# Optimization experiments

Measured on AMD Instinct MI355X. Metric: run time of the kernel, lower is better.

Reference implementation:

```python
import jax, jax.numpy as jnp
import numpy as np

B, N, CQ, CKV, CP = 4, 1024, 128, 64, 16
H, NB = 4, 3
D = CQ // H  # 32 per-head dim
NQ, NK = 32, 128
CENTRES = 15.5 + 32.0 * np.arange(N // NQ)  # subset centres covering all atoms


def _ln(x, eps=1e-5):
    m = jnp.mean(x, axis=-1, keepdims=True)
    v = jnp.var(x, axis=-1, keepdims=True)
    return (x - m) * jax.lax.rsqrt(v + eps)


def _adaln(a, s, s_gamma, w_gate, w_skip):
    # AF3 AdaLN: a normalized without affine, modulated by conditioning s
    a_n = _ln(a)
    s_n = _ln(s) * s_gamma
    return jax.nn.sigmoid(s_n @ w_gate) * a_n + s_n @ w_skip


def _local_bias():
    # sequence-local block mask (union over subset centres), Algorithm 7
    idx = jnp.arange(N, dtype=jnp.float32)
    cen = jnp.asarray(CENTRES, dtype=jnp.float32)
    lcond = jnp.abs(idx[None, :] - cen[:, None]) < NQ / 2  # [C, N] query window
    mcond = jnp.abs(idx[None, :] - cen[:, None]) < NK / 2  # [C, N] key window
    cond = jnp.any(lcond[:, :, None] & mcond[:, None, :], axis=0)  # [N, N]
    return jnp.where(cond, 0.0, -1e10)


def _forward(q, c, p, attn_s_gamma, attn_gate_w, attn_skip_w, attn_wq, attn_bq,
             attn_wk, attn_wv, attn_lnz_g, attn_lnz_b, attn_wb, attn_wgate,
             attn_wo, attn_ws_out, attn_bs_out, trans_s_gamma, trans_gate_w,
             trans_skip_w, trans_w1, trans_w2, trans_wout, trans_ws_out,
             trans_bs_out):
    beta = _local_bias()  # [N, N]
    inv_sqrt_d = 1.0 / np.sqrt(D)
    a = q
    for i in range(NB):  # 3 structurally distinct blocks
        # --- AttentionPairBias (AF3 Alg 24) ---
        ah = _adaln(a, c, attn_s_gamma[i], attn_gate_w[i], attn_skip_w[i])
        qh = (ah @ attn_wq[i] + attn_bq[i]).reshape(B, N, H, D)
        kh = (ah @ attn_wk[i]).reshape(B, N, H, D)
        vh = (ah @ attn_wv[i]).reshape(B, N, H, D)
        zb = (_ln(p) * attn_lnz_g[i] + attn_lnz_b[i]) @ attn_wb[i]  # [B,N,N,H]
        bias = jnp.transpose(zb, (0, 3, 1, 2)) + beta[None, None]  # [B,H,N,N]
        scores = jnp.einsum('bqhd,bkhd->bhqk', qh, kh) * inv_sqrt_d + bias
        w = jax.nn.softmax(scores, axis=-1)
        o = jnp.einsum('bhqk,bkhd->bqhd', w, vh)
        g = jax.nn.sigmoid((ah @ attn_wgate[i]).reshape(B, N, H, D))
        o = (g * o).reshape(B, N, CQ) @ attn_wo[i]
        attn_out = jax.nn.sigmoid(c @ attn_ws_out[i] + attn_bs_out[i]) * o
        # --- ConditionedTransitionBlock (AF3 Alg 25, n=2 SwiGLU) ---
        t = _adaln(a, c, trans_s_gamma[i], trans_gate_w[i], trans_skip_w[i])
        bm = jax.nn.silu(t @ trans_w1[i]) * (t @ trans_w2[i])
        t_out = jax.nn.sigmoid(c @ trans_ws_out[i] + trans_bs_out[i]) * (bm @ trans_wout[i])
        # AF3 Alg 23: a <- attn_out + transition(a, s)
        a = attn_out + t_out
    return a


def setup_inputs() -> dict:
    key = jax.random.key(0)
    ks = iter(jax.random.split(key, 64))

    def rnd(shape, scale=0.02):
        return jax.random.normal(next(ks), shape, dtype=jnp.float32) * scale

    return {
        'q': jax.random.normal(next(ks), (B, N, CQ), dtype=jnp.float32),
        'c': jax.random.normal(next(ks), (B, N, CKV), dtype=jnp.float32),
        'p': jax.random.normal(next(ks), (B, N, N, CP), dtype=jnp.float32),
        'attn_s_gamma': jnp.ones((NB, CKV), jnp.float32),
        'attn_gate_w': rnd((NB, CKV, CQ)),
        'attn_skip_w': rnd((NB, CKV, CQ)),
        'attn_wq': rnd((NB, CQ, CQ)),
        'attn_bq': jnp.zeros((NB, CQ), jnp.float32),
        'attn_wk': rnd((NB, CQ, CQ)),
        'attn_wv': rnd((NB, CQ, CQ)),
        'attn_lnz_g': jnp.ones((NB, CP), jnp.float32),
        'attn_lnz_b': jnp.zeros((NB, CP), jnp.float32),
        'attn_wb': rnd((NB, CP, H)),
        'attn_wgate': rnd((NB, CQ, CQ)),
        'attn_wo': rnd((NB, CQ, CQ)),
        'attn_ws_out': rnd((NB, CKV, CQ)),
        'attn_bs_out': jnp.full((NB, CQ), -2.0, jnp.float32),
        'trans_s_gamma': jnp.ones((NB, CKV), jnp.float32),
        'trans_gate_w': rnd((NB, CKV, CQ)),
        'trans_skip_w': rnd((NB, CKV, CQ)),
        'trans_w1': rnd((NB, CQ, 2 * CQ)),
        'trans_w2': rnd((NB, CQ, 2 * CQ)),
        'trans_wout': rnd((NB, 2 * CQ, CQ)),
        'trans_ws_out': rnd((NB, CKV, CQ)),
        'trans_bs_out': jnp.full((NB, CQ), -2.0, jnp.float32),
    }


def reference(q, c, p, attn_s_gamma, attn_gate_w, attn_skip_w, attn_wq, attn_bq,
              attn_wk, attn_wv, attn_lnz_g, attn_lnz_b, attn_wb, attn_wgate,
              attn_wo, attn_ws_out, attn_bs_out, trans_s_gamma, trans_gate_w,
              trans_skip_w, trans_w1, trans_w2, trans_wout, trans_ws_out,
              trans_bs_out):
    return _forward(q, c, p, attn_s_gamma, attn_gate_w, attn_skip_w, attn_wq,
                    attn_bq, attn_wk, attn_wv, attn_lnz_g, attn_lnz_b, attn_wb,
                    attn_wgate, attn_wo, attn_ws_out, attn_bs_out,
                    trans_s_gamma, trans_gate_w, trans_skip_w, trans_w1,
                    trans_w2, trans_wout, trans_ws_out, trans_bs_out)
```

## Files before the change

### kernel.cpp

```cpp
#include <hip/hip_runtime.h>
#include <math.h>

#define NB_ 3
#define B_ 4
#define N_ 1024
#define CQ_ 128
#define CKV_ 64
#define CP_ 16
#define H_ 4
#define D_ 32
#define R_ (B_*N_)
#define KW_ 128

__device__ __forceinline__ float sigmoidf_(float x) {
    return 1.0f / (1.0f + __expf(-x));
}

#define AN_OFF 0
#define SA_OFF 1056
#define ST_OFF 1600
#define CR_OFF 2144
#define TH_OFF 2688
#define SCR_OFF 3744
#define SMEM_F (3744 + 6336)

__global__ __launch_bounds__(512, 4) void k_pre(
    const float* __restrict__ a, const float* __restrict__ c,
    const float* __restrict__ a_sg, const float* __restrict__ a_gw,
    const float* __restrict__ a_sw, const float* __restrict__ a_wso,
    const float* __restrict__ a_bso,
    const float* __restrict__ t_sg, const float* __restrict__ t_gw,
    const float* __restrict__ t_sw, const float* __restrict__ t_wso,
    const float* __restrict__ t_bso,
    const float* __restrict__ wq, const float* __restrict__ bq,
    const float* __restrict__ wk, const float* __restrict__ wv,
    const float* __restrict__ wg,
    const float* __restrict__ w1, const float* __restrict__ w2,
    float* __restrict__ qh, float* __restrict__ kh,
    float* __restrict__ vh, float* __restrict__ gh,
    float* __restrict__ bm,
    float* __restrict__ asig, float* __restrict__ tsig)
{
    __shared__ float smem[SMEM_F];
    const int t = threadIdx.x;
    const int base = blockIdx.x * 8;

    {
        const int rloc = t >> 6, li = t & 63;
        const int row = base + rloc;
        float2 av = *(const float2*)(a + row * 128 + li * 2);
        float s = av.x + av.y;
        float ss = av.x * av.x + av.y * av.y;
        float cv = c[row * 64 + li];
        float cs = cv, css = cv * cv;
        #pragma unroll
        for (int m = 1; m < 64; m <<= 1) {
            s += __shfl_xor(s, m);
            ss += __shfl_xor(ss, m);
            cs += __shfl_xor(cs, m);
            css += __shfl_xor(css, m);
        }
        const float am = s * (1.0f / 128.0f);
        const float ars = rsqrtf(ss * (1.0f / 128.0f) - am * am + 1e-5f);
        const float cm = cs * (1.0f / 64.0f);
        const float crs = rsqrtf(css * (1.0f / 64.0f) - cm * cm + 1e-5f);
        smem[AN_OFF + rloc * 132 + li * 2]     = (av.x - am) * ars;
        smem[AN_OFF + rloc * 132 + li * 2 + 1] = (av.y - am) * ars;
        const float cn = (cv - cm) * crs;
        smem[SA_OFF + rloc * 68 + li] = cn * a_sg[li];
        smem[ST_OFF + rloc * 68 + li] = cn * t_sg[li];
        smem[CR_OFF + rloc * 68 + li] = cv;
    }
    __syncthreads();

    const int wave = t >> 6;
    const int lane = t & 63;
    const int ig = lane >> 4;
    const int jc = lane & 15;
    const int c0 = jc * 8;
    const int r0 = ig * 2, r1 = ig * 2 + 1;

    if (wave < 6) {
        const float* W;
        const float* xs;
        switch (wave) {
            case 0: W = a_gw;  xs = smem + SA_OFF; break;
            case 1: W = a_sw;  xs = smem + SA_OFF; break;
            case 2: W = t_gw;  xs = smem + ST_OFF; break;
            case 3: W = t_sw;  xs = smem + ST_OFF; break;
            case 4: W = a_wso; xs = smem + CR_OFF; break;
            default: W = t_wso; xs = smem + CR_OFF; break;
        }
        W += c0;
        float acc0[8], acc1[8];
        #pragma unroll
        for (int e = 0; e < 8; e++) { acc0[e] = 0.f; acc1[e] = 0.f; }
        for (int kk = 0; kk < 64; kk += 4) {
            float4 x40 = *(const float4*)(xs + r0 * 68 + kk);
            float4 x41 = *(const float4*)(xs + r1 * 68 + kk);
            #pragma unroll
            for (int q = 0; q < 4; q++) {
                const float4 wlo = *(const float4*)(W + (kk + q) * 128);
                const float4 whi = *(const float4*)(W + (kk + q) * 128 + 4);
                const float xa = ((const float*)&x40)[q];
                const float xb = ((const float*)&x41)[q];
                acc0[0] += xa * wlo.x; acc0[1] += xa * wlo.y;
                acc0[2] += xa * wlo.z; acc0[3] += xa * wlo.w;
                acc0[4] += xa * whi.x; acc0[5] += xa * whi.y;
                acc0[6] += xa * whi.z; acc0[7] += xa * whi.w;
                acc1[0] += xb * wlo.x; acc1[1] += xb * wlo.y;
                acc1[2] += xb * wlo.z; acc1[3] += xb * wlo.w;
                acc1[4] += xb * whi.x; acc1[5] += xb * whi.y;
                acc1[6] += xb * whi.z; acc1[7] += xb * whi.w;
            }
        }
        float* sc = smem + SCR_OFF + wave * 1056;
        *(float4*)(sc + r0 * 132 + c0)     = make_float4(acc0[0], acc0[1], acc0[2], acc0[3]);
        *(float4*)(sc + r0 * 132 + c0 + 4) = make_float4(acc0[4], acc0[5], acc0[6], acc0[7]);
        *(float4*)(sc + r1 * 132 + c0)     = make_float4(acc1[0], acc1[1], acc1[2], acc1[3]);
        *(float4*)(sc + r1 * 132 + c0 + 4) = make_float4(acc1[4], acc1[5], acc1[6], acc1[7]);
    }
    __syncthreads();

    #pragma unroll
    for (int i2 = 0; i2 < 2; i2++) {
        const int e = t + i2 * 512;
        const int r = e >> 7, cc = e & 127;
        const float* sc = smem + SCR_OFF + r * 132 + cc;
        const float anv = smem[AN_OFF + r * 132 + cc];
        const float ahv = sigmoidf_(sc[0]) * anv + sc[1056];
        const float thv = sigmoidf_(sc[2 * 1056]) * anv + sc[3 * 1056];
        smem[AN_OFF + r * 132 + cc] = ahv;
        smem[TH_OFF + r * 132 + cc] = thv;
        const int idx = (base + r) * 128 + cc;
        asig[idx] = sigmoidf_(sc[4 * 1056] + a_bso[cc]);
        tsig[idx] = sigmoidf_(sc[5 * 1056] + t_bso[cc]);
    }
    __syncthreads();

    {
        const float* W;
        const float* xs;
        int ldw, sel2 = 0, cb = 0;
        if (wave < 4) {
            W = (wave == 0 ? wq : wave == 1 ? wk : wave == 2 ? wv : wg) + c0;
            xs = smem + AN_OFF;
            ldw = 128;
        } else {
            const int u = (wave - 4) * 128 + c0;
            sel2 = u >> 8; cb = u & 255;
            W = (sel2 ? w2 : w1) + cb;
            xs = smem + TH_OFF;
            ldw = 256;
        }
        float acc0[8], acc1[8];
        #pragma unroll
        for (int e = 0; e < 8; e++) {
            const float init = (wave == 0) ? bq[c0 + e] : 0.f;
            acc0[e] = init; acc1[e] = init;
        }
        for (int kk = 0; kk < 128; kk += 4) {
            float4 x40 = *(const float4*)(xs + r0 * 132 + kk);
            float4 x41 = *(const float4*)(xs + r1 * 132 + kk);
            #pragma unroll
            for (int q = 0; q < 4; q++) {
                const float4 wlo = *(const float4*)(W + (kk + q) * ldw);
                const float4 whi = *(const float4*)(W + (kk + q) * ldw + 4);
                const float xa = ((const float*)&x40)[q];
                const float xb = ((const float*)&x41)[q];
                acc0[0] += xa * wlo.x; acc0[1] += xa * wlo.y;
                acc0[2] += xa * wlo.z; acc0[3] += xa * wlo.w;
                acc0[4] += xa * whi.x; acc0[5] += xa * whi.y;
                acc0[6] += xa * whi.z; acc0[7] += xa * whi.w;
                acc1[0] += xb * wlo.x; acc1[1] += xb * wlo.y;
                acc1[2] += xb * wlo.z; acc1[3] += xb * wlo.w;
                acc1[4] += xb * whi.x; acc1[5] += xb * whi.y;
                acc1[6] += xb * whi.z; acc1[7] += xb * whi.w;
            }
        }
        if (wave < 4) {
            float* dst = (wave == 0 ? qh : wave == 1 ? kh : wave == 2 ? vh : gh);
            if (wave == 3) {
                #pragma unroll
                for (int e = 0; e < 8; e++) {
                    acc0[e] = sigmoidf_(acc0[e]);
                    acc1[e] = sigmoidf_(acc1[e]);
                }
            }
            *(float4*)(dst + (base + r0) * 128 + c0)     = make_float4(acc0[0], acc0[1], acc0[2], acc0[3]);
            *(float4*)(dst + (base + r0) * 128 + c0 + 4) = make_float4(acc0[4], acc0[5], acc0[6], acc0[7]);
            *(float4*)(dst + (base + r1) * 128 + c0)     = make_float4(acc1[0], acc1[1], acc1[2], acc1[3]);
            *(float4*)(dst + (base + r1) * 128 + c0 + 4) = make_float4(acc1[4], acc1[5], acc1[6], acc1[7]);
        } else {
            float* bsc = smem + SCR_OFF + sel2 * 2080;
            *(float4*)(bsc + r0 * 260 + cb)     = make_float4(acc0[0], acc0[1], acc0[2], acc0[3]);
            *(float4*)(bsc + r0 * 260 + cb + 4) = make_float4(acc0[4], acc0[5], acc0[6], acc0[7]);
            *(float4*)(bsc + r1 * 260 + cb)     = make_float4(acc1[0], acc1[1], acc1[2], acc1[3]);
            *(float4*)(bsc + r1 * 260 + cb + 4) = make_float4(acc1[4], acc1[5], acc1[6], acc1[7]);
        }
    }
    __syncthreads();

    #pragma unroll
    for (int i2 = 0; i2 < 4; i2++) {
        const int e = t + i2 * 512;
        const int r = e >> 8, cc = e & 255;
        const float a1 = smem[SCR_OFF + r * 260 + cc];
        const float a2 = smem[SCR_OFF + 2080 + r * 260 + cc];
        bm[(base + r) * 256 + cc] = a1 * sigmoidf_(a1) * a2;
    }
}

__global__ __launch_bounds__(256) void k_zbias(
    const float* __restrict__ p,
    const float* __restrict__ lnz_g, const float* __restrict__ lnz_b,
    const float* __restrict__ wb, float* __restrict__ zb)
{
    const int tid = blockIdx.x * 256 + threadIdx.x;
    const int kk = tid & 127;
    const int n = (tid >> 7) & 1023;
    const int b = tid >> 17;
    const int row = b * N_ + n;
    const int k = ((n >> 5) << 5) - 48 + kk;

    if (k < 0 || k >= N_) {
        #pragma unroll
        for (int blk = 0; blk < NB_; blk++) {
            float* zo = zb + ((size_t)(blk * R_ + row) * H_) * KW_ + kk;
            #pragma unroll
            for (int h = 0; h < H_; h++) zo[h * KW_] = -1e10f;
        }
        return;
    }
    const float* pp = p + ((size_t)row * N_ + k) * CP_;
    float pv[16];
    float4 p0 = *(const float4*)(pp);
    float4 p1 = *(const float4*)(pp + 4);
    float4 p2 = *(const float4*)(pp + 8);
    float4 p3 = *(const float4*)(pp + 12);
    pv[0]=p0.x; pv[1]=p0.y; pv[2]=p0.z; pv[3]=p0.w;
    pv[4]=p1.x; pv[5]=p1.y; pv[6]=p1.z; pv[7]=p1.w;
    pv[8]=p2.x; pv[9]=p2.y; pv[10]=p2.z; pv[11]=p2.w;
    pv[12]=p3.x; pv[13]=p3.y; pv[14]=p3.z; pv[15]=p3.w;
    float s = 0.f, ss = 0.f;
    #pragma unroll
    for (int i = 0; i < 16; i++) { s += pv[i]; ss += pv[i] * pv[i]; }
    const float m = s * (1.0f / 16.0f);
    const float rs = rsqrtf(ss * (1.0f / 16.0f) - m * m + 1e-5f);

    #pragma unroll
    for (int blk = 0; blk < NB_; blk++) {
        const float* g = lnz_g + blk * 16;
        const float* bb = lnz_b + blk * 16;
        const float* w = wb + blk * 64;
        float z0 = 0.f, z1 = 0.f, z2 = 0.f, z3 = 0.f;
        #pragma unroll
        for (int cp = 0; cp < 16; cp++) {
            const float val = (pv[cp] - m) * rs * g[cp] + bb[cp];
            z0 += val * w[cp * 4 + 0];
            z1 += val * w[cp * 4 + 1];
            z2 += val * w[cp * 4 + 2];
            z3 += val * w[cp * 4 + 3];
        }
        float* zo = zb + ((size_t)(blk * R_ + row) * H_) * KW_ + kk;
        zo[0] = z0; zo[KW_] = z1; zo[2 * KW_] = z2; zo[3 * KW_] = z3;
    }
}

__global__ __launch_bounds__(256) void k_attn(
    const float* __restrict__ qh, const float* __restrict__ kh,
    const float* __restrict__ vh, const float* __restrict__ gh,
    const float* __restrict__ zb, float* __restrict__ og)
{
    __shared__ float kT[32][136];
    __shared__ float vs[128][36];
    __shared__ float wsm[32][132];

    const int t = threadIdx.x;
    const int qb = blockIdx.x, h = blockIdx.y, b = blockIdx.z;
    const int k0 = qb * 32 - 48;

    #pragma unroll
    for (int i = 0; i < 4; i++) {
        const int e = t + i * 256;
        const int kk = e >> 3, d4 = (e & 7) * 4;
        const int kg = k0 + kk;
        float4 kv = make_float4(0.f, 0.f, 0.f, 0.f);
        float4 vv = make_float4(0.f, 0.f, 0.f, 0.f);
        if (kg >= 0 && kg < N_) {
            const int addr = (b * N_ + kg) * 128 + h * 32 + d4;
            kv = *(const float4*)(kh + addr);
            vv = *(const float4*)(vh + addr);
        }
        kT[d4 + 0][kk] = kv.x;
        kT[d4 + 1][kk] = kv.y;
        kT[d4 + 2][kk] = kv.z;
        kT[d4 + 3][kk] = kv.w;
        *(float4*)&vs[kk][d4] = vv;
    }

    const int q = t >> 3, j = t & 7;
    const int n = qb * 32 + q;
    const float* qrow = qh + (b * N_ + n) * 128 + h * 32;
    float4 qf[8];
    #pragma unroll
    for (int dq = 0; dq < 8; dq++) qf[dq] = *(const float4*)(qrow + dq * 4);
    const float* zrow = zb + ((size_t)(b * N_ + n) * H_ + h) * KW_;
    float4 zf[4];
    #pragma unroll
    for (int g4 = 0; g4 < 4; g4++) zf[g4] = *(const float4*)(zrow + g4 * 32 + j * 4);
    __syncthreads();

    float4 acc[4];
    #pragma unroll
    for (int g4 = 0; g4 < 4; g4++) acc[g4] = make_float4(0.f, 0.f, 0.f, 0.f);
    const float* qfs = (const float*)qf;
    #pragma unroll
    for (int d = 0; d < 32; d++) {
        const float qd = qfs[d];
        #pragma unroll
        for (int g4 = 0; g4 < 4; g4++) {
            const float4 k4 = *(const float4*)&kT[d][g4 * 32 + j * 4];
            acc[g4].x += qd * k4.x; acc[g4].y += qd * k4.y;
            acc[g4].z += qd * k4.z; acc[g4].w += qd * k4.w;
        }
    }
    const float scale = 0.1767766952966369f;
    float fr[16];
    #pragma unroll
    for (int g4 = 0; g4 < 4; g4++) {
        fr[g4*4+0] = zf[g4].x + acc[g4].x * scale;
        fr[g4*4+1] = zf[g4].y + acc[g4].y * scale;
        fr[g4*4+2] = zf[g4].z + acc[g4].z * scale;
        fr[g4*4+3] = zf[g4].w + acc[g4].w * scale;
    }
    float mx = fr[0];
    #pragma unroll
    for (int i = 1; i < 16; i++) mx = fmaxf(mx, fr[i]);
    #pragma unroll
    for (int mk = 1; mk < 8; mk <<= 1) mx = fmaxf(mx, __shfl_xor(mx, mk));
    float sum = 0.f;
    #pragma unroll
    for (int i = 0; i < 16; i++) { fr[i] = __expf(fr[i] - mx); sum += fr[i]; }
    #pragma unroll
    for (int mk = 1; mk < 8; mk <<= 1) sum += __shfl_xor(sum, mk);
    const float rinv = 1.0f / sum;
    #pragma unroll
    for (int g4 = 0; g4 < 4; g4++) {
        *(float4*)&wsm[q][g4 * 32 + j * 4] = make_float4(
            fr[g4*4+0] * rinv, fr[g4*4+1] * rinv,
            fr[g4*4+2] * rinv, fr[g4*4+3] * rinv);
    }
    asm volatile("s_waitcnt lgkmcnt(0)" ::: "memory");

    const int addrO = (b * N_ + n) * 128 + h * 32 + j * 4;
    const float4 g4v = *(const float4*)(gh + addrO);
    float4 o = make_float4(0.f, 0.f, 0.f, 0.f);
    #pragma unroll 4
    for (int kk = 0; kk < 128; kk += 4) {
        const float4 w4 = *(const float4*)&wsm[q][kk];
        const float4 v0 = *(const float4*)&vs[kk + 0][j * 4];
        const float4 v1 = *(const float4*)&vs[kk + 1][j * 4];
        const float4 v2 = *(const float4*)&vs[kk + 2][j * 4];
        const float4 v3 = *(const float4*)&vs[kk + 3][j * 4];
        o.x += w4.x * v0.x + w4.y * v1.x + w4.z * v2.x + w4.w * v3.x;
        o.y += w4.x * v0.y + w4.y * v1.y + w4.z * v2.y + w4.w * v3.y;
        o.z += w4.x * v0.z + w4.y * v1.z + w4.z * v2.z + w4.w * v3.z;
        o.w += w4.x * v0.w + w4.y * v1.w + w4.z * v2.w + w4.w * v3.w;
    }
    float4 outv;
    outv.x = o.x * g4v.x; outv.y = o.y * g4v.y;
    outv.z = o.z * g4v.z; outv.w = o.w * g4v.w;
    *(float4*)(og + addrO) = outv;
}

__global__ __launch_bounds__(256, 4) void k_combine(
    const float* __restrict__ og, const float* __restrict__ bm,
    const float* __restrict__ wo, const float* __restrict__ wout,
    const float* __restrict__ asig, const float* __restrict__ tsig,
    float* __restrict__ out)
{
    __shared__ float scr[4 * 1056];
    const int t = threadIdx.x;
    const int base = blockIdx.x * 8;
    const int wave = t >> 6, lane = t & 63;
    const int ig = lane >> 4, jc = lane & 15;
    const int c0 = jc * 8;
    const int r0 = ig * 2, r1 = ig * 2 + 1;

    float acc0[8], acc1[8];
    #pragma unroll
    for (int e = 0; e < 8; e++) { acc0[e] = 0.f; acc1[e] = 0.f; }

    if (wave < 2) {
        const float* W = wo + c0;
        const float* X = og + base * 128;
        const int kbeg = wave * 64;
        for (int kk = kbeg; kk < kbeg + 64; kk += 4) {
            float4 x40 = *(const float4*)(X + r0 * 128 + kk);
            float4 x41 = *(const float4*)(X + r1 * 128 + kk);
            #pragma unroll
            for (int q = 0; q < 4; q++) {
                const float4 wlo = *(const float4*)(W + (kk + q) * 128);
                const float4 whi = *(const float4*)(W + (kk + q) * 128 + 4);
                const float xa = ((const float*)&x40)[q];
                const float xb = ((const float*)&x41)[q];
                acc0[0] += xa * wlo.x; acc0[1] += xa * wlo.y;
                acc0[2] += xa * wlo.z; acc0[3] += xa * wlo.w;
                acc0[4] += xa * whi.x; acc0[5] += xa * whi.y;
                acc0[6] += xa * whi.z; acc0[7] += xa * whi.w;
                acc1[0] += xb * wlo.x; acc1[1] += xb * wlo.y;
                acc1[2] += xb * wlo.z; acc1[3] += xb * wlo.w;
                acc1[4] += xb * whi.x; acc1[5] += xb * whi.y;
                acc1[6] += xb * whi.z; acc1[7] += xb * whi.w;
            }
        }
    } else {
        const float* W = wout + c0;
        const float* X = bm + base * 256;
        const int kbeg = (wave - 2) * 128;
        for (int kk = kbeg; kk < kbeg + 128; kk += 4) {
            float4 x40 = *(const float4*)(X + r0 * 256 + kk);
            float4 x41 = *(const float4*)(X + r1 * 256 + kk);
            #pragma unroll
            for (int q = 0; q < 4; q++) {
                const float4 wlo = *(const float4*)(W + (kk + q) * 128);
                const float4 whi = *(const float4*)(W + (kk + q) * 128 + 4);
                const float xa = ((const float*)&x40)[q];
                const float xb = ((const float*)&x41)[q];
                acc0[0] += xa * wlo.x; acc0[1] += xa * wlo.y;
                acc0[2] += xa * wlo.z; acc0[3] += xa * wlo.w;
                acc0[4] += xa * whi.x; acc0[5] += xa * whi.y;
                acc0[6] += xa * whi.z; acc0[7] += xa * whi.w;
                acc1[0] += xb * wlo.x; acc1[1] += xb * wlo.y;
                acc1[2] += xb * wlo.z; acc1[3] += xb * wlo.w;
                acc1[4] += xb * whi.x; acc1[5] += xb * whi.y;
                acc1[6] += xb * whi.z; acc1[7] += xb * whi.w;
            }
        }
    }
    float* sc = scr + wave * 1056;
    *(float4*)(sc + r0 * 132 + c0)     = make_float4(acc0[0], acc0[1], acc0[2], acc0[3]);
    *(float4*)(sc + r0 * 132 + c0 + 4) = make_float4(acc0[4], acc0[5], acc0[6], acc0[7]);
    *(float4*)(sc + r1 * 132 + c0)     = make_float4(acc1[0], acc1[1], acc1[2], acc1[3]);
    *(float4*)(sc + r1 * 132 + c0 + 4) = make_float4(acc1[4], acc1[5], acc1[6], acc1[7]);
    __syncthreads();

    #pragma unroll
    for (int i2 = 0; i2 < 4; i2++) {
        const int e = t + i2 * 256;
        const int r = e >> 7, cc = e & 127;
        const float* s = scr + r * 132 + cc;
        const int idx = (base + r) * 128 + cc;
        out[idx] = asig[idx] * (s[0] + s[1056]) + tsig[idx] * (s[2112] + s[3168]);
    }
}

extern "C" void kernel_launch(void* const* d_in, const int* in_sizes, int n_in,
                              void* d_out, int out_size, void* d_ws, size_t ws_size,
                              hipStream_t stream)
{
    const float* q        = (const float*)d_in[0];
    const float* c        = (const float*)d_in[1];
    const float* p        = (const float*)d_in[2];
    const float* a_sg_all = (const float*)d_in[3];
    const float* a_gw_all = (const float*)d_in[4];
    const float* a_sw_all = (const float*)d_in[5];
    const float* wq_all   = (const float*)d_in[6];
    const float* bq_all   = (const float*)d_in[7];
    const float* wk_all   = (const float*)d_in[8];
    const float* wv_all   = (const float*)d_in[9];
    const float* lnzg_all = (const float*)d_in[10];
    const float* lnzb_all = (const float*)d_in[11];
    const float* wb_all   = (const float*)d_in[12];
    const float* wgt_all  = (const float*)d_in[13];
    const float* wo_all   = (const float*)d_in[14];
    const float* awso_all = (const float*)d_in[15];
    const float* abso_all = (const float*)d_in[16];
    const float* t_sg_all = (const float*)d_in[17];
    const float* t_gw_all = (const float*)d_in[18];
    const float* t_sw_all = (const float*)d_in[19];
    const float* w1_all   = (const float*)d_in[20];
    const float* w2_all   = (const float*)d_in[21];
    const float* wout_all = (const float*)d_in[22];
    const float* twso_all = (const float*)d_in[23];
    const float* tbso_all = (const float*)d_in[24];

    float* ws = (float*)d_ws;
    const size_t RC = (size_t)R_ * CQ_;
    float* qh   = ws;
    float* kh   = ws + RC;
    float* vh   = ws + 2 * RC;
    float* gh   = ws + 3 * RC;
    float* bmb  = ws + 4 * RC;
    float* asig = ws + 6 * RC;
    float* tsig = ws + 7 * RC;
    float* abuf = ws + 8 * RC;
    float* ogb  = ws + 9 * RC;
    float* zbb  = ws + 10 * RC;

    k_zbias<<<dim3(B_ * N_ * KW_ / 256), dim3(256), 0, stream>>>(
        p, lnzg_all, lnzb_all, wb_all, zbb);

    const float* acur = q;
    for (int blk = 0; blk < NB_; blk++) {
        k_pre<<<dim3(R_ / 8), dim3(512), 0, stream>>>(
            acur, c,
            a_sg_all + blk * CKV_, a_gw_all + blk * CKV_ * CQ_,
            a_sw_all + blk * CKV_ * CQ_, awso_all + blk * CKV_ * CQ_,
            abso_all + blk * CQ_,
            t_sg_all + blk * CKV_, t_gw_all + blk * CKV_ * CQ_,
            t_sw_all + blk * CKV_ * CQ_, twso_all + blk * CKV_ * CQ_,
            tbso_all + blk * CQ_,
            wq_all + blk * CQ_ * CQ_, bq_all + blk * CQ_,
            wk_all + blk * CQ_ * CQ_, wv_all + blk * CQ_ * CQ_,
            wgt_all + blk * CQ_ * CQ_,
            w1_all + blk * CQ_ * 2 * CQ_, w2_all + blk * CQ_ * 2 * CQ_,
            qh, kh, vh, gh, bmb, asig, tsig);
        k_attn<<<dim3(N_ / 32, H_, B_), dim3(256), 0, stream>>>(
            qh, kh, vh, gh, zbb + (size_t)blk * R_ * H_ * KW_, ogb);
        float* outp = (blk == NB_ - 1) ? (float*)d_out : abuf;
        k_combine<<<dim3(R_ / 8), dim3(256), 0, stream>>>(
            ogb, bmb, wo_all + blk * CQ_ * CQ_, wout_all + blk * 2 * CQ_ * CQ_,
            asig, tsig, outp);
        acur = abuf;
    }
}
```

Before: 631.2 us.

## Fuse block output combine with next block's AdaLN and projections

Merges the per-block combine kernel (Wo and Wout projections with gated residual) into the next block's pre-processing kernel, so the intermediate activation stays in shared memory instead of round-tripping through global memory. A separate final kernel handles the last block. This removes one launch per block and the write and read of the activation buffer. In exchange the fused kernel uses more shared memory and 512 threads with an occupancy hint, which could reduce occupancy.

```diff
diff --git a/kernel.cpp b/kernel.cpp
--- a/kernel.cpp
+++ b/kernel.cpp
@@ -211,192 +211,309 @@
     }
 }
 
-__global__ __launch_bounds__(256) void k_zbias(
-    const float* __restrict__ p,
-    const float* __restrict__ lnz_g, const float* __restrict__ lnz_b,
-    const float* __restrict__ wb, float* __restrict__ zb)
+#define C_AN 0
+#define C_TH 1056
+#define C_SA 2112
+#define C_ST 2656
+#define C_CR 3200
+#define C_SCR 3744
+#define C_SMEM (3744 + 8448)
+
+__global__ __launch_bounds__(512, 4) void k_cpre(
+    const float* __restrict__ og, float* __restrict__ bmio,
+    const float* __restrict__ wo, const float* __restrict__ wout,
+    float* __restrict__ asig, float* __restrict__ tsig,
+    const float* __restrict__ c,
+    const float* __restrict__ a_sg, const float* __restrict__ a_gw,
+    const float* __restrict__ a_sw, const float* __restrict__ a_wso,
+    const float* __restrict__ a_bso,
+    const float* __restrict__ t_sg, const float* __restrict__ t_gw,
+    const float* __restrict__ t_sw, const float* __restrict__ t_wso,
+    const float* __restrict__ t_bso,
+    const float* __restrict__ wq, const float* __restrict__ bq,
+    const float* __restrict__ wk, const float* __restrict__ wv,
+    const float* __restrict__ wg,
+    const float* __restrict__ w1, const float* __restrict__ w2,
+    float* __restrict__ qh, float* __restrict__ kh,
+    float* __restrict__ vh, float* __restrict__ gh)
 {
-    const int tid = blockIdx.x * 256 + threadIdx.x;
-    const int kk = tid & 127;
-    const int n = (tid >> 7) & 1023;
-    const int b = tid >> 17;
-    const int row = b * N_ + n;
-    const int k = ((n >> 5) << 5) - 48 + kk;
-
-    if (k < 0 || k >= N_) {
-        #pragma unroll
-        for (int blk = 0; blk < NB_; blk++) {
-            float* zo = zb + ((size_t)(blk * R_ + row) * H_) * KW_ + kk;
+    __shared__ float smem[C_SMEM];
+    const int t = threadIdx.x;
+    const int base = blockIdx.x * 8;
+    const int wave = t >> 6, lane = t & 63;
+    const int ig = lane >> 4, jc = lane & 15;
+    const int c0 = jc * 8;
+    const int r0 = ig * 2, r1 = r0 + 1;
+
+    const int rloc = wave, li = lane;
+    const float cv  = c[(base + rloc) * 64 + li];
+    const float sgA = a_sg[li], sgT = t_sg[li];
+    const int e1 = t + 512;
+    const int br0 = t >> 7,  bc0 = t & 127;
+    const int br1 = e1 >> 7, bc1 = e1 & 127;
+    const int gidx0 = (base + br0) * 128 + bc0;
+    const int gidx1 = (base + br1) * 128 + bc1;
+    const float as0 = asig[gidx0], ts0 = tsig[gidx0];
+    const float as1 = asig[gidx1], ts1 = tsig[gidx1];
+
+    {
+        float acc0[8], acc1[8];
+        #pragma unroll
+        for (int e = 0; e < 8; e++) { acc0[e] = 0.f; acc1[e] = 0.f; }
+        if (wave < 4) {
+            const float* W = wo + c0;
+            const float* X = og + base * 128;
+            const int kbeg = wave * 32;
+            for (int kk = kbeg; kk < kbeg + 32; kk += 4) {
+                float4 x40 = *(const float4*)(X + r0 * 128 + kk);
+                float4 x41 = *(const float4*)(X + r1 * 128 + kk);
+                #pragma unroll
+                for (int q = 0; q < 4; q++) {
+                    const float4 wlo = *(const float4*)(W + (kk + q) * 128);
+                    const float4 whi = *(const float4*)(W + (kk + q) * 128 + 4);
+                    const float xa = ((const float*)&x40)[q];
+                    const float xb = ((const float*)&x41)[q];
+                    acc0[0] += xa * wlo.x; acc0[1] += xa * wlo.y;
+                    acc0[2] += xa * wlo.z; acc0[3] += xa * wlo.w;
+                    acc0[4] += xa * whi.x; acc0[5] += xa * whi.y;
+                    acc0[6] += xa * whi.z; acc0[7] += xa * whi.w;
+                    acc1[0] += xb * wlo.x; acc1[1] += xb * wlo.y;
+                    acc1[2] += xb * wlo.z; acc1[3] += xb * wlo.w;
+                    acc1[4] += xb * whi.x; acc1[5] += xb * whi.y;
+                    acc1[6] += xb * whi.z; acc1[7] += xb * whi.w;
+                }
+            }
+        } else {
+            const float* W = wout + c0;
+            const float* X = bmio + base * 256;
+            const int kbeg = (wave - 4) * 64;
+            for (int kk = kbeg; kk < kbeg + 64; kk += 4) {
+                float4 x40 = *(const float4*)(X + r0 * 256 + kk);
+                float4 x41 = *(const float4*)(X + r1 * 256 + kk);
+                #pragma unroll
+                for (int q = 0; q < 4; q++) {
+                    const float4 wlo = *(const float4*)(W + (kk + q) * 128);
+                    const float4 whi = *(const float4*)(W + (kk + q) * 128 + 4);
+                    const float xa = ((const float*)&x40)[q];
+                    const float xb = ((const float*)&x41)[q];
+                    acc0[0] += xa * wlo.x; acc0[1] += xa * wlo.y;
+                    acc0[2] += xa * wlo.z; acc0[3] += xa * wlo.w;
+                    acc0[4] += xa * whi.x; acc0[5] += xa * whi.y;
+                    acc0[6] += xa * whi.z; acc0[7] += xa * whi.w;
+                    acc1[0] += xb * wlo.x; acc1[1] += xb * wlo.y;
+                    acc1[2] += xb * wlo.z; acc1[3] += xb * wlo.w;
+                    acc1[4] += xb * whi.x; acc1[5] += xb * whi.y;
+                    acc1[6] += xb * whi.z; acc1[7] += xb * whi.w;
+                }
+            }
+        }
+        float* sc = smem + C_SCR + wave * 1056;
+        *(float4*)(sc + r0 * 132 + c0)     = make_float4(acc0[0], acc0[1], acc0[2], acc0[3]);
+        *(float4*)(sc + r0 * 132 + c0 + 4) = make_float4(acc0[4], acc0[5], acc0[6], acc0[7]);
+        *(float4*)(sc + r1 * 132 + c0)     = make_float4(acc1[0], acc1[1], acc1[2], acc1[3]);
+        *(float4*)(sc + r1 * 132 + c0 + 4) = make_float4(acc1[4], acc1[5], acc1[6], acc1[7]);
+    }
+    __syncthreads();
+
+    {
+        const float* s0 = smem + C_SCR + br0 * 132 + bc0;
+        const float so0 = s0[0] + s0[1056] + s0[2112] + s0[3168];
+        const float st0 = s0[4224] + s0[5280] + s0[6336] + s0[7392];
+        smem[C_AN + br0 * 132 + bc0] = as0 * so0 + ts0 * st0;
+        const float* s1 = smem + C_SCR + br1 * 132 + bc1;
+        const float so1 = s1[0] + s1[1056] + s1[2112] + s1[3168];
+        const float st1 = s1[4224] + s1[5280] + s1[6336] + s1[7392];
+        smem[C_AN + br1 * 132 + bc1] = as1 * so1 + ts1 * st1;
+    }
+    __syncthreads();
+
+    {
+        float2 av = *(const float2*)&smem[C_AN + rloc * 132 + li * 2];
+        float s = av.x + av.y;
+        float ss = av.x * av.x + av.y * av.y;
+        float cs = cv, css = cv * cv;
+        #pragma unroll
+        for (int m = 1; m < 64; m <<= 1) {
+            s += __shfl_xor(s, m);
+            ss += __shfl_xor(ss, m);
+            cs += __shfl_xor(cs, m);
+            css += __shfl_xor(css, m);
+        }
+        const float am = s * (1.0f / 128.0f);
+        const float ars = rsqrtf(ss * (1.0f / 128.0f) - am * am + 1e-5f);
+        const float cm = cs * (1.0f / 64.0f);
+        const float crs = rsqrtf(css * (1.0f / 64.0f) - cm * cm + 1e-5f);
+        smem[C_AN + rloc * 132 + li * 2]     = (av.x - am) * ars;
+        smem[C_AN + rloc * 132 + li * 2 + 1] = (av.y - am) * ars;
+        const float cn = (cv - cm) * crs;
+        smem[C_SA + rloc * 68 + li] = cn * sgA;
+        smem[C_ST + rloc * 68 + li] = cn * sgT;
+        smem[C_CR + rloc * 68 + li] = cv;
+    }
+    __syncthreads();
+
+    if (wave < 6) {
+        const float* W;
+        const float* xs;
+        switch (wave) {
+            case 0: W = a_gw;  xs = smem + C_SA; break;
+            case 1: W = a_sw;  xs = smem + C_SA; break;
+            case 2: W = t_gw;  xs = smem + C_ST; break;
+            case 3: W = t_sw;  xs = smem + C_ST; break;
+            case 4: W = a_wso; xs = smem + C_CR; break;
+            default: W = t_wso; xs = smem + C_CR; break;
+        }
+        W += c0;
+        float acc0[8], acc1[8];
+        #pragma unroll
+        for (int e = 0; e < 8; e++) { acc0[e] = 0.f; acc1[e] = 0.f; }
+        for (int kk = 0; kk < 64; kk += 4) {
+            float4 x40 = *(const float4*)(xs + r0 * 68 + kk);
+            float4 x41 = *(const float4*)(xs + r1 * 68 + kk);
             #pragma unroll
-            for (int h = 0; h < H_; h++) zo[h * KW_] = -1e10f;
-        }
-        return;
-    }
-    const float* pp = p + ((size_t)row * N_ + k) * CP_;
-    float pv[16];
-    float4 p0 = *(const float4*)(pp);
-    float4 p1 = *(const float4*)(pp + 4);
-    float4 p2 = *(const float4*)(pp + 8);
-    float4 p3 = *(const float4*)(pp + 12);
-    pv[0]=p0.x; pv[1]=p0.y; pv[2]=p0.z; pv[3]=p0.w;
-    pv[4]=p1.x; pv[5]=p1.y; pv[6]=p1.z; pv[7]=p1.w;
-    pv[8]=p2.x; pv[9]=p2.y; pv[10]=p2.z; pv[11]=p2.w;
-    pv[12]=p3.x; pv[13]=p3.y; pv[14]=p3.z; pv[15]=p3.w;
-    float s = 0.f, ss = 0.f;
-    #pragma unroll
-    for (int i = 0; i < 16; i++) { s += pv[i]; ss += pv[i] * pv[i]; }
-    const float m = s * (1.0f / 16.0f);
-    const float rs = rsqrtf(ss * (1.0f / 16.0f) - m * m + 1e-5f);
-
-    #pragma unroll
-    for (int blk = 0; blk < NB_; blk++) {
-        const float* g = lnz_g + blk * 16;
-        const float* bb = lnz_b + blk * 16;
-        const float* w = wb + blk * 64;
-        float z0 = 0.f, z1 = 0.f, z2 = 0.f, z3 = 0.f;
-        #pragma unroll
-        for (int cp = 0; cp < 16; cp++) {
-            const float val = (pv[cp] - m) * rs * g[cp] + bb[cp];
-            z0 += val * w[cp * 4 + 0];
-            z1 += val * w[cp * 4 + 1];
-            z2 += val * w[cp * 4 + 2];
-            z3 += val * w[cp * 4 + 3];
-        }
-        float* zo = zb + ((size_t)(blk * R_ + row) * H_) * KW_ + kk;
-        zo[0] = z0; zo[KW_] = z1; zo[2 * KW_] = z2; zo[3 * KW_] = z3;
+            for (int q = 0; q < 4; q++) {
+                const float4 wlo = *(const float4*)(W + (kk + q) * 128);
+                const float4 whi = *(const float4*)(W + (kk + q) * 128 + 4);
+                const float xa = ((const float*)&x40)[q];
+                const float xb = ((const float*)&x41)[q];
+                acc0[0] += xa * wlo.x; acc0[1] += xa * wlo.y;
+                acc0[2] += xa * wlo.z; acc0[3] += xa * wlo.w;
+                acc0[4] += xa * whi.x; acc0[5] += xa * whi.y;
+                acc0[6] += xa * whi.z; acc0[7] += xa * whi.w;
+                acc1[0] += xb * wlo.x; acc1[1] += xb * wlo.y;
+                acc1[2] += xb * wlo.z; acc1[3] += xb * wlo.w;
+                acc1[4] += xb * whi.x; acc1[5] += xb * whi.y;
+                acc1[6] += xb * whi.z; acc1[7] += xb * whi.w;
+            }
+        }
+        float* sc = smem + C_SCR + wave * 1056;
+        *(float4*)(sc + r0 * 132 + c0)     = make_float4(acc0[0], acc0[1], acc0[2], acc0[3]);
+        *(float4*)(sc + r0 * 132 + c0 + 4) = make_float4(acc0[4], acc0[5], acc0[6], acc0[7]);
+        *(float4*)(sc + r1 * 132 + c0)     = make_float4(acc1[0], acc1[1], acc1[2], acc1[3]);
+        *(float4*)(sc + r1 * 132 + c0 + 4) = make_float4(acc1[4], acc1[5], acc1[6], acc1[7]);
+    }
+    __syncthreads();
+
+    #pragma unroll
+    for (int i2 = 0; i2 < 2; i2++) {
+        const int e = t + i2 * 512;
+        const int r = e >> 7, cc = e & 127;
+        const float* sc = smem + C_SCR + r * 132 + cc;
+        const float anv = smem[C_AN + r * 132 + cc];
+        const float ahv = sigmoidf_(sc[0]) * anv + sc[1056];
+        const float thv = sigmoidf_(sc[2 * 1056]) * anv + sc[3 * 1056];
+        smem[C_AN + r * 132 + cc] = ahv;
+        smem[C_TH + r * 132 + cc] = thv;
+        const int idx = (base + r) * 128 + cc;
+        asig[idx] = sigmoidf_(sc[4 * 1056] + a_bso[cc]);
+        tsig[idx] = sigmoidf_(sc[5 * 1056] + t_bso[cc]);
+    }
+    __syncthreads();
+
+    {
+        const float* W;
+        const float* xs;
+        int ldw, sel2 = 0, cb = 0;
+        if (wave < 4) {
+            W = (wave == 0 ? wq : wave == 1 ? wk : wave == 2 ? wv : wg) + c0;
+            xs = smem + C_AN;
+            ldw = 128;
+        } else {
+            const int u = (wave - 4) * 128 + c0;
+            sel2 = u >> 8; cb = u & 255;
+            W = (sel2 ? w2 : w1) + cb;
+            xs = smem + C_TH;
+            ldw = 256;
+        }
+        float acc0[8], acc1[8];
+        #pragma unroll
+        for (int e = 0; e < 8; e++) {
+            const float init = (wave == 0) ? bq[c0 + e] : 0.f;
+            acc0[e] = init; acc1[e] = init;
+        }
+        for (int kk = 0; kk < 128; kk += 4) {
+            float4 x40 = *(const float4*)(xs + r0 * 132 + kk);
+            float4 x41 = *(const float4*)(xs + r1 * 132 + kk);
+            #pragma unroll
+            for (int q = 0; q < 4; q++) {
+                const float4 wlo = *(const float4*)(W + (kk + q) * ldw);
+                const float4 whi = *(const float4*)(W + (kk + q) * ldw + 4);
+                const float xa = ((const float*)&x40)[q];
+                const float xb = ((const float*)&x41)[q];
+                acc0[0] += xa * wlo.x; acc0[1] += xa * wlo.y;
+                acc0[2] += xa * wlo.z; acc0[3] += xa * wlo.w;
+                acc0[4] += xa * whi.x; acc0[5] += xa * whi.y;
+                acc0[6] += xa * whi.z; acc0[7] += xa * whi.w;
+                acc1[0] += xb * wlo.x; acc1[1] += xb * wlo.y;
+                acc1[2] += xb * wlo.z; acc1[3] += xb * wlo.w;
+                acc1[4] += xb * whi.x; acc1[5] += xb * whi.y;
+                acc1[6] += xb * whi.z; acc1[7] += xb * whi.w;
+            }
+        }
+        if (wave < 4) {
+            float* dst = (wave == 0 ? qh : wave == 1 ? kh : wave == 2 ? vh : gh);
+            if (wave == 3) {
+                #pragma unroll
+                for (int e = 0; e < 8; e++) {
+                    acc0[e] = sigmoidf_(acc0[e]);
+                    acc1[e] = sigmoidf_(acc1[e]);
+                }
+            }
+            *(float4*)(dst + (base + r0) * 128 + c0)     = make_float4(acc0[0], acc0[1], acc0[2], acc0[3]);
+            *(float4*)(dst + (base + r0) * 128 + c0 + 4) = make_float4(acc0[4], acc0[5], acc0[6], acc0[7]);
+            *(float4*)(dst + (base + r1) * 128 + c0)     = make_float4(acc1[0], acc1[1], acc1[2], acc1[3]);
+            *(float4*)(dst + (base + r1) * 128 + c0 + 4) = make_float4(acc1[4], acc1[5], acc1[6], acc1[7]);
+        } else {
+            float* bsc = smem + C_SCR + sel2 * 2080;
+            *(float4*)(bsc + r0 * 260 + cb)     = make_float4(acc0[0], acc0[1], acc0[2], acc0[3]);
+            *(float4*)(bsc + r0 * 260 + cb + 4) = make_float4(acc0[4], acc0[5], acc0[6], acc0[7]);
+            *(float4*)(bsc + r1 * 260 + cb)     = make_float4(acc1[0], acc1[1], acc1[2], acc1[3]);
+            *(float4*)(bsc + r1 * 260 + cb + 4) = make_float4(acc1[4], acc1[5], acc1[6], acc1[7]);
+        }
+    }
+    __syncthreads();
+
+    #pragma unroll
+    for (int i2 = 0; i2 < 4; i2++) {
+        const int e = t + i2 * 512;
+        const int r = e >> 8, cc = e & 255;
+        const float a1 = smem[C_SCR + r * 260 + cc];
+        const float a2 = smem[C_SCR + 2080 + r * 260 + cc];
+        bmio[(base + r) * 256 + cc] = a1 * sigmoidf_(a1) * a2;
     }
 }
 
-__global__ __launch_bounds__(256) void k_attn(
-    const float* __restrict__ qh, const float* __restrict__ kh,
-    const float* __restrict__ vh, const float* __restrict__ gh,
-    const float* __restrict__ zb, float* __restrict__ og)
-{
-    __shared__ float kT[32][136];
-    __shared__ float vs[128][36];
-    __shared__ float wsm[32][132];
-
-    const int t = threadIdx.x;
-    const int qb = blockIdx.x, h = blockIdx.y, b = blockIdx.z;
-    const int k0 = qb * 32 - 48;
-
-    #pragma unroll
-    for (int i = 0; i < 4; i++) {
-        const int e = t + i * 256;
-        const int kk = e >> 3, d4 = (e & 7) * 4;
-        const int kg = k0 + kk;
-        float4 kv = make_float4(0.f, 0.f, 0.f, 0.f);
-        float4 vv = make_float4(0.f, 0.f, 0.f, 0.f);
-        if (kg >= 0 && kg < N_) {
-            const int addr = (b * N_ + kg) * 128 + h * 32 + d4;
-            kv = *(const float4*)(kh + addr);
-            vv = *(const float4*)(vh + addr);
-        }
-        kT[d4 + 0][kk] = kv.x;
-        kT[d4 + 1][kk] = kv.y;
-        kT[d4 + 2][kk] = kv.z;
-        kT[d4 + 3][kk] = kv.w;
-        *(float4*)&vs[kk][d4] = vv;
-    }
-
-    const int q = t >> 3, j = t & 7;
-    const int n = qb * 32 + q;
-    const float* qrow = qh + (b * N_ + n) * 128 + h * 32;
-    float4 qf[8];
-    #pragma unroll
-    for (int dq = 0; dq < 8; dq++) qf[dq] = *(const float4*)(qrow + dq * 4);
-    const float* zrow = zb + ((size_t)(b * N_ + n) * H_ + h) * KW_;
-    float4 zf[4];
-    #pragma unroll
-    for (int g4 = 0; g4 < 4; g4++) zf[g4] = *(const float4*)(zrow + g4 * 32 + j * 4);
-    __syncthreads();
-
-    float4 acc[4];
-    #pragma unroll
-    for (int g4 = 0; g4 < 4; g4++) acc[g4] = make_float4(0.f, 0.f, 0.f, 0.f);
-    const float* qfs = (const float*)qf;
-    #pragma unroll
-    for (int d = 0; d < 32; d++) {
-        const float qd = qfs[d];
-        #pragma unroll
-        for (int g4 = 0; g4 < 4; g4++) {
-            const float4 k4 = *(const float4*)&kT[d][g4 * 32 + j * 4];
-            acc[g4].x += qd * k4.x; acc[g4].y += qd * k4.y;
-            acc[g4].z += qd * k4.z; acc[g4].w += qd * k4.w;
-        }
-    }
-    const float scale = 0.1767766952966369f;
-    float fr[16];
-    #pragma unroll
-    for (int g4 = 0; g4 < 4; g4++) {
-        fr[g4*4+0] = zf[g4].x + acc[g4].x * scale;
-        fr[g4*4+1] = zf[g4].y + acc[g4].y * scale;
-        fr[g4*4+2] = zf[g4].z + acc[g4].z * scale;
-        fr[g4*4+3] = zf[g4].w + acc[g4].w * scale;
-    }
-    float mx = fr[0];
-    #pragma unroll
-    for (int i = 1; i < 16; i++) mx = fmaxf(mx, fr[i]);
-    #pragma unroll
-    for (int mk = 1; mk < 8; mk <<= 1) mx = fmaxf(mx, __shfl_xor(mx, mk));
-    float sum = 0.f;
-    #pragma unroll
-    for (int i = 0; i < 16; i++) { fr[i] = __expf(fr[i] - mx); sum += fr[i]; }
-    #pragma unroll
-    for (int mk = 1; mk < 8; mk <<= 1) sum += __shfl_xor(sum, mk);
-    const float rinv = 1.0f / sum;
-    #pragma unroll
-    for (int g4 = 0; g4 < 4; g4++) {
-        *(float4*)&wsm[q][g4 * 32 + j * 4] = make_float4(
-            fr[g4*4+0] * rinv, fr[g4*4+1] * rinv,
-            fr[g4*4+2] * rinv, fr[g4*4+3] * rinv);
-    }
-    asm volatile("s_waitcnt lgkmcnt(0)" ::: "memory");
-
-    const int addrO = (b * N_ + n) * 128 + h * 32 + j * 4;
-    const float4 g4v = *(const float4*)(gh + addrO);
-    float4 o = make_float4(0.f, 0.f, 0.f, 0.f);
-    #pragma unroll 4
-    for (int kk = 0; kk < 128; kk += 4) {
-        const float4 w4 = *(const float4*)&wsm[q][kk];
-        const float4 v0 = *(const float4*)&vs[kk + 0][j * 4];
-        const float4 v1 = *(const float4*)&vs[kk + 1][j * 4];
-        const float4 v2 = *(const float4*)&vs[kk + 2][j * 4];
-        const float4 v3 = *(const float4*)&vs[kk + 3][j * 4];
-        o.x += w4.x * v0.x + w4.y * v1.x + w4.z * v2.x + w4.w * v3.x;
-        o.y += w4.x * v0.y + w4.y * v1.y + w4.z * v2.y + w4.w * v3.y;
-        o.z += w4.x * v0.z + w4.y * v1.z + w4.z * v2.z + w4.w * v3.z;
-        o.w += w4.x * v0.w + w4.y * v1.w + w4.z * v2.w + w4.w * v3.w;
-    }
-    float4 outv;
-    outv.x = o.x * g4v.x; outv.y = o.y * g4v.y;
-    outv.z = o.z * g4v.z; outv.w = o.w * g4v.w;
-    *(float4*)(og + addrO) = outv;
-}
-
-__global__ __launch_bounds__(256, 4) void k_combine(
+__global__ __launch_bounds__(512, 4) void k_fin(
     const float* __restrict__ og, const float* __restrict__ bm,
     const float* __restrict__ wo, const float* __restrict__ wout,
     const float* __restrict__ asig, const float* __restrict__ tsig,
     float* __restrict__ out)
 {
-    __shared__ float scr[4 * 1056];
+    __shared__ float scr[8 * 1056];
     const int t = threadIdx.x;
     const int base = blockIdx.x * 8;
     const int wave = t >> 6, lane = t & 63;
     const int ig = lane >> 4, jc = lane & 15;
     const int c0 = jc * 8;
-    const int r0 = ig * 2, r1 = ig * 2 + 1;
+    const int r0 = ig * 2, r1 = r0 + 1;
+
+    const int e1 = t + 512;
+    const int br0 = t >> 7,  bc0 = t & 127;
+    const int br1 = e1 >> 7, bc1 = e1 & 127;
+    const int gidx0 = (base + br0) * 128 + bc0;
+    const int gidx1 = (base + br1) * 128 + bc1;
+    const float as0 = asig[gidx0], ts0 = tsig[gidx0];
+    const float as1 = asig[gidx1], ts1 = tsig[gidx1];
 
     float acc0[8], acc1[8];
     #pragma unroll
     for (int e = 0; e < 8; e++) { acc0[e] = 0.f; acc1[e] = 0.f; }
 
-    if (wave < 2) {
+    if (wave < 4) {
         const float* W = wo + c0;
         const float* X = og + base * 128;
-        const int kbeg = wave * 64;
-        for (int kk = kbeg; kk < kbeg + 64; kk += 4) {
+        const int kbeg = wave * 32;
+        for (int kk = kbeg; kk < kbeg + 32; kk += 4) {
             float4 x40 = *(const float4*)(X + r0 * 128 + kk);
             float4 x41 = *(const float4*)(X + r1 * 128 + kk);
             #pragma unroll
@@ -418,8 +535,8 @@
     } else {
         const float* W = wout + c0;
         const float* X = bm + base * 256;
-        const int kbeg = (wave - 2) * 128;
-        for (int kk = kbeg; kk < kbeg + 128; kk += 4) {
+        const int kbeg = (wave - 4) * 64;
+        for (int kk = kbeg; kk < kbeg + 64; kk += 4) {
             float4 x40 = *(const float4*)(X + r0 * 256 + kk);
             float4 x41 = *(const float4*)(X + r1 * 256 + kk);
             #pragma unroll
@@ -446,14 +563,177 @@
     *(float4*)(sc + r1 * 132 + c0 + 4) = make_float4(acc1[4], acc1[5], acc1[6], acc1[7]);
     __syncthreads();
 
-    #pragma unroll
-    for (int i2 = 0; i2 < 4; i2++) {
-        const int e = t + i2 * 256;
-        const int r = e >> 7, cc = e & 127;
-        const float* s = scr + r * 132 + cc;
-        const int idx = (base + r) * 128 + cc;
-        out[idx] = asig[idx] * (s[0] + s[1056]) + tsig[idx] * (s[2112] + s[3168]);
-    }
+    {
+        const float* s0 = scr + br0 * 132 + bc0;
+        out[gidx0] = as0 * (s0[0] + s0[1056] + s0[2112] + s0[3168])
+                   + ts0 * (s0[4224] + s0[5280] + s0[6336] + s0[7392]);
+        const float* s1 = scr + br1 * 132 + bc1;
+        out[gidx1] = as1 * (s1[0] + s1[1056] + s1[2112] + s1[3168])
+                   + ts1 * (s1[4224] + s1[5280] + s1[6336] + s1[7392]);
+    }
+}
+
+__global__ __launch_bounds__(256) void k_zbias(
+    const float* __restrict__ p,
+    const float* __restrict__ lnz_g, const float* __restrict__ lnz_b,
+    const float* __restrict__ wb, float* __restrict__ zb)
+{
+    const int tid = blockIdx.x * 256 + threadIdx.x;
+    const int kk = tid & 127;
+    const int n = (tid >> 7) & 1023;
+    const int b = tid >> 17;
+    const int row = b * N_ + n;
+    const int k = ((n >> 5) << 5) - 48 + kk;
+
+    if (k < 0 || k >= N_) {
+        #pragma unroll
+        for (int blk = 0; blk < NB_; blk++) {
+            float* zo = zb + ((size_t)(blk * R_ + row) * H_) * KW_ + kk;
+            #pragma unroll
+            for (int h = 0; h < H_; h++) zo[h * KW_] = -1e10f;
+        }
+        return;
+    }
+    const float* pp = p + ((size_t)row * N_ + k) * CP_;
+    float pv[16];
+    float4 p0 = *(const float4*)(pp);
+    float4 p1 = *(const float4*)(pp + 4);
+    float4 p2 = *(const float4*)(pp + 8);
+    float4 p3 = *(const float4*)(pp + 12);
+    pv[0]=p0.x; pv[1]=p0.y; pv[2]=p0.z; pv[3]=p0.w;
+    pv[4]=p1.x; pv[5]=p1.y; pv[6]=p1.z; pv[7]=p1.w;
+    pv[8]=p2.x; pv[9]=p2.y; pv[10]=p2.z; pv[11]=p2.w;
+    pv[12]=p3.x; pv[13]=p3.y; pv[14]=p3.z; pv[15]=p3.w;
+    float s = 0.f, ss = 0.f;
+    #pragma unroll
+    for (int i = 0; i < 16; i++) { s += pv[i]; ss += pv[i] * pv[i]; }
+    const float m = s * (1.0f / 16.0f);
+    const float rs = rsqrtf(ss * (1.0f / 16.0f) - m * m + 1e-5f);
+
+    #pragma unroll
+    for (int blk = 0; blk < NB_; blk++) {
+        const float* g = lnz_g + blk * 16;
+        const float* bb = lnz_b + blk * 16;
+        const float* w = wb + blk * 64;
+        float z0 = 0.f, z1 = 0.f, z2 = 0.f, z3 = 0.f;
+        #pragma unroll
+        for (int cp = 0; cp < 16; cp++) {
+            const float val = (pv[cp] - m) * rs * g[cp] + bb[cp];
+            z0 += val * w[cp * 4 + 0];
+            z1 += val * w[cp * 4 + 1];
+            z2 += val * w[cp * 4 + 2];
+            z3 += val * w[cp * 4 + 3];
+        }
+        float* zo = zb + ((size_t)(blk * R_ + row) * H_) * KW_ + kk;
+        zo[0] = z0; zo[KW_] = z1; zo[2 * KW_] = z2; zo[3 * KW_] = z3;
+    }
+}
+
+__global__ __launch_bounds__(256) void k_attn(
+    const float* __restrict__ qh, const float* __restrict__ kh,
+    const float* __restrict__ vh, const float* __restrict__ gh,
+    const float* __restrict__ zb, float* __restrict__ og)
+{
+    __shared__ float kT[32][136];
+    __shared__ float vs[128][36];
+    __shared__ float wsm[32][132];
+
+    const int t = threadIdx.x;
+    const int qb = blockIdx.x, h = blockIdx.y, b = blockIdx.z;
+    const int k0 = qb * 32 - 48;
+
+    #pragma unroll
+    for (int i = 0; i < 4; i++) {
+        const int e = t + i * 256;
+        const int kk = e >> 3, d4 = (e & 7) * 4;
+        const int kg = k0 + kk;
+        float4 kv = make_float4(0.f, 0.f, 0.f, 0.f);
+        float4 vv = make_float4(0.f, 0.f, 0.f, 0.f);
+        if (kg >= 0 && kg < N_) {
+            const int addr = (b * N_ + kg) * 128 + h * 32 + d4;
+            kv = *(const float4*)(kh + addr);
+            vv = *(const float4*)(vh + addr);
+        }
+        kT[d4 + 0][kk] = kv.x;
+        kT[d4 + 1][kk] = kv.y;
+        kT[d4 + 2][kk] = kv.z;
+        kT[d4 + 3][kk] = kv.w;
+        *(float4*)&vs[kk][d4] = vv;
+    }
+
+    const int q = t >> 3, j = t & 7;
+    const int n = qb * 32 + q;
+    const float* qrow = qh + (b * N_ + n) * 128 + h * 32;
+    float4 qf[8];
+    #pragma unroll
+    for (int dq = 0; dq < 8; dq++) qf[dq] = *(const float4*)(qrow + dq * 4);
+    const float* zrow = zb + ((size_t)(b * N_ + n) * H_ + h) * KW_;
+    float4 zf[4];
+    #pragma unroll
+    for (int g4 = 0; g4 < 4; g4++) zf[g4] = *(const float4*)(zrow + g4 * 32 + j * 4);
+    __syncthreads();
+
+    float4 acc[4];
+    #pragma unroll
+    for (int g4 = 0; g4 < 4; g4++) acc[g4] = make_float4(0.f, 0.f, 0.f, 0.f);
+    const float* qfs = (const float*)qf;
+    #pragma unroll
+    for (int d = 0; d < 32; d++) {
+        const float qd = qfs[d];
+        #pragma unroll
+        for (int g4 = 0; g4 < 4; g4++) {
+            const float4 k4 = *(const float4*)&kT[d][g4 * 32 + j * 4];
+            acc[g4].x += qd * k4.x; acc[g4].y += qd * k4.y;
+            acc[g4].z += qd * k4.z; acc[g4].w += qd * k4.w;
+        }
+    }
+    const float scale = 0.1767766952966369f;
+    float fr[16];
+    #pragma unroll
+    for (int g4 = 0; g4 < 4; g4++) {
+        fr[g4*4+0] = zf[g4].x + acc[g4].x * scale;
+        fr[g4*4+1] = zf[g4].y + acc[g4].y * scale;
+        fr[g4*4+2] = zf[g4].z + acc[g4].z * scale;
+        fr[g4*4+3] = zf[g4].w + acc[g4].w * scale;
+    }
+    float mx = fr[0];
+    #pragma unroll
+    for (int i = 1; i < 16; i++) mx = fmaxf(mx, fr[i]);
+    #pragma unroll
+    for (int mk = 1; mk < 8; mk <<= 1) mx = fmaxf(mx, __shfl_xor(mx, mk));
+    float sum = 0.f;
+    #pragma unroll
+    for (int i = 0; i < 16; i++) { fr[i] = __expf(fr[i] - mx); sum += fr[i]; }
+    #pragma unroll
+    for (int mk = 1; mk < 8; mk <<= 1) sum += __shfl_xor(sum, mk);
+    const float rinv = 1.0f / sum;
+    #pragma unroll
+    for (int g4 = 0; g4 < 4; g4++) {
+        *(float4*)&wsm[q][g4 * 32 + j * 4] = make_float4(
+            fr[g4*4+0] * rinv, fr[g4*4+1] * rinv,
+            fr[g4*4+2] * rinv, fr[g4*4+3] * rinv);
+    }
+    asm volatile("s_waitcnt lgkmcnt(0)" ::: "memory");
+
+    const int addrO = (b * N_ + n) * 128 + h * 32 + j * 4;
+    const float4 g4v = *(const float4*)(gh + addrO);
+    float4 o = make_float4(0.f, 0.f, 0.f, 0.f);
+    #pragma unroll 4
+    for (int kk = 0; kk < 128; kk += 4) {
+        const float4 w4 = *(const float4*)&wsm[q][kk];
+        const float4 v0 = *(const float4*)&vs[kk + 0][j * 4];
+        const float4 v1 = *(const float4*)&vs[kk + 1][j * 4];
+        const float4 v2 = *(const float4*)&vs[kk + 2][j * 4];
+        const float4 v3 = *(const float4*)&vs[kk + 3][j * 4];
+        o.x += w4.x * v0.x + w4.y * v1.x + w4.z * v2.x + w4.w * v3.x;
+        o.y += w4.x * v0.y + w4.y * v1.y + w4.z * v2.y + w4.w * v3.y;
+        o.z += w4.x * v0.z + w4.y * v1.z + w4.z * v2.z + w4.w * v3.z;
+        o.w += w4.x * v0.w + w4.y * v1.w + w4.z * v2.w + w4.w * v3.w;
+    }
+    float4 outv;
+    outv.x = o.x * g4v.x; outv.y = o.y * g4v.y;
+    outv.z = o.z * g4v.z; outv.w = o.w * g4v.w;
+    *(float4*)(og + addrO) = outv;
 }
 
 extern "C" void kernel_launch(void* const* d_in, const int* in_sizes, int n_in,
@@ -495,34 +775,45 @@
     float* bmb  = ws + 4 * RC;
     float* asig = ws + 6 * RC;
     float* tsig = ws + 7 * RC;
-    float* abuf = ws + 8 * RC;
-    float* ogb  = ws + 9 * RC;
-    float* zbb  = ws + 10 * RC;
+    float* ogb  = ws + 8 * RC;
+    float* zbb  = ws + 9 * RC;
 
     k_zbias<<<dim3(B_ * N_ * KW_ / 256), dim3(256), 0, stream>>>(
         p, lnzg_all, lnzb_all, wb_all, zbb);
 
-    const float* acur = q;
+    k_pre<<<dim3(R_ / 8), dim3(512), 0, stream>>>(
+        q, c,
+        a_sg_all, a_gw_all, a_sw_all, awso_all, abso_all,
+        t_sg_all, t_gw_all, t_sw_all, twso_all, tbso_all,
+        wq_all, bq_all, wk_all, wv_all, wgt_all,
+        w1_all, w2_all,
+        qh, kh, vh, gh, bmb, asig, tsig);
+
     for (int blk = 0; blk < NB_; blk++) {
-        k_pre<<<dim3(R_ / 8), dim3(512), 0, stream>>>(
-            acur, c,
-            a_sg_all + blk * CKV_, a_gw_all + blk * CKV_ * CQ_,
-            a_sw_all + blk * CKV_ * CQ_, awso_all + blk * CKV_ * CQ_,
-            abso_all + blk * CQ_,
-            t_sg_all + blk * CKV_, t_gw_all + blk * CKV_ * CQ_,
-            t_sw_all + blk * CKV_ * CQ_, twso_all + blk * CKV_ * CQ_,
-            tbso_all + blk * CQ_,
-            wq_all + blk * CQ_ * CQ_, bq_all + blk * CQ_,
-            wk_all + blk * CQ_ * CQ_, wv_all + blk * CQ_ * CQ_,
-            wgt_all + blk * CQ_ * CQ_,
-            w1_all + blk * CQ_ * 2 * CQ_, w2_all + blk * CQ_ * 2 * CQ_,
-            qh, kh, vh, gh, bmb, asig, tsig);
         k_attn<<<dim3(N_ / 32, H_, B_), dim3(256), 0, stream>>>(
             qh, kh, vh, gh, zbb + (size_t)blk * R_ * H_ * KW_, ogb);
-        float* outp = (blk == NB_ - 1) ? (float*)d_out : abuf;
-        k_combine<<<dim3(R_ / 8), dim3(256), 0, stream>>>(
-            ogb, bmb, wo_all + blk * CQ_ * CQ_, wout_all + blk * 2 * CQ_ * CQ_,
-            asig, tsig, outp);
-        acur = abuf;
+        if (blk < NB_ - 1) {
+            const int nx = blk + 1;
+            k_cpre<<<dim3(R_ / 8), dim3(512), 0, stream>>>(
+                ogb, bmb,
+                wo_all + blk * CQ_ * CQ_, wout_all + blk * 2 * CQ_ * CQ_,
+                asig, tsig, c,
+                a_sg_all + nx * CKV_, a_gw_all + nx * CKV_ * CQ_,
+                a_sw_all + nx * CKV_ * CQ_, awso_all + nx * CKV_ * CQ_,
+                abso_all + nx * CQ_,
+                t_sg_all + nx * CKV_, t_gw_all + nx * CKV_ * CQ_,
+                t_sw_all + nx * CKV_ * CQ_, twso_all + nx * CKV_ * CQ_,
+                tbso_all + nx * CQ_,
+                wq_all + nx * CQ_ * CQ_, bq_all + nx * CQ_,
+                wk_all + nx * CQ_ * CQ_, wv_all + nx * CQ_ * CQ_,
+                wgt_all + nx * CQ_ * CQ_,
+                w1_all + nx * CQ_ * 2 * CQ_, w2_all + nx * CQ_ * 2 * CQ_,
+                qh, kh, vh, gh);
+        } else {
+            k_fin<<<dim3(R_ / 8), dim3(512), 0, stream>>>(
+                ogb, bmb,
+                wo_all + blk * CQ_ * CQ_, wout_all + blk * 2 * CQ_ * CQ_,
+                asig, tsig, (float*)d_out);
+        }
     }
 }
```

After: 582.0 us. 7.8% less time.
